# Kernel optimization log

Measured on AMD Instinct MI355X. Metric: run time of the kernel, lower is better.

Reference implementation:

```python
import jax, jax.numpy as jnp
import numpy as np

NUM_HEADS = 16
THETA = 10000.0


def _rope(x, cos, sin):
    # x: [B, H, S, d_k]; cos/sin: [S, d_k//2]
    x_even = x[..., 0::2]
    x_odd = x[..., 1::2]
    out_even = x_even * cos - x_odd * sin
    out_odd = x_odd * cos + x_even * sin
    # interleave back to original even/odd layout
    return jnp.stack([out_even, out_odd], axis=-1).reshape(x.shape)


def setup_inputs() -> dict:
    key = jax.random.key(0)
    ks = jax.random.split(key, 5)
    B, S, D = 2, 2048, 1024
    std = 2.0 / (D + D)
    return {
        "x": jax.random.normal(ks[0], (B, S, D), dtype=jnp.float32),
        "w_q": jax.random.normal(ks[1], (D, D), dtype=jnp.float32) * std,
        "w_k": jax.random.normal(ks[2], (D, D), dtype=jnp.float32) * std,
        "w_v": jax.random.normal(ks[3], (D, D), dtype=jnp.float32) * std,
        "w_o": jax.random.normal(ks[4], (D, D), dtype=jnp.float32) * std,
    }


def reference(x, w_q, w_k, w_v, w_o):
    B, S, D = x.shape
    H = NUM_HEADS
    d_k = D // H

    # QKV projections: x @ W.T
    q = jnp.einsum('bsd,ed->bse', x, w_q).reshape(B, S, H, d_k).transpose(0, 2, 1, 3)
    k = jnp.einsum('bsd,ed->bse', x, w_k).reshape(B, S, H, d_k).transpose(0, 2, 1, 3)
    v = jnp.einsum('bsd,ed->bse', x, w_v).reshape(B, S, H, d_k).transpose(0, 2, 1, 3)

    # RoPE (token_positions = arange(S))
    pos = jnp.arange(S, dtype=jnp.float32)
    inv_freq = 1.0 / (THETA ** (2.0 * jnp.arange(d_k // 2, dtype=jnp.float32) / d_k))
    angles = pos[:, None] * inv_freq[None, :]  # [S, d_k//2]
    cos, sin = jnp.cos(angles), jnp.sin(angles)
    q = _rope(q, cos, sin)
    k = _rope(k, cos, sin)

    # causal attention
    scores = jnp.einsum('bhqd,bhkd->bhqk', q, k) / jnp.sqrt(jnp.float32(d_k))
    causal = jnp.tril(jnp.ones((S, S), dtype=bool))
    scores = jnp.where(causal[None, None], scores, -jnp.inf)
    attn = jax.nn.softmax(scores, axis=-1)
    out = jnp.einsum('bhqk,bhkd->bhqd', attn, v)  # [B, H, S, d_k]

    out = out.transpose(0, 2, 1, 3).reshape(B, S, D)
    return jnp.einsum('bsd,ed->bse', out, w_o)
```

## Files before the change

kernel.cpp:

```cpp
#include <hip/hip_runtime.h>

typedef unsigned short u16;
typedef unsigned int u32;
typedef short bf16x8 __attribute__((ext_vector_type(8)));
typedef float f32x4 __attribute__((ext_vector_type(4)));

#define CSC 0.18033688011112042f

__device__ __forceinline__ u16 f2bf(float f) {
    union { float f; unsigned u; } x; x.f = f;
    unsigned r = x.u + 0x7fffu + ((x.u >> 16) & 1u);
    return (u16)(r >> 16);
}
__device__ __forceinline__ float bf2f(u16 v) {
    union { unsigned u; float f; } x; x.u = ((unsigned)v) << 16;
    return x.f;
}
__device__ __forceinline__ float exp2_fast(float x) {
#if __has_builtin(__builtin_amdgcn_exp2f)
    return __builtin_amdgcn_exp2f(x);
#else
    return exp2f(x);
#endif
}
__device__ __forceinline__ void gl_lds16(const u16* g, u16* l) {
#if __has_builtin(__builtin_amdgcn_global_load_lds)
    __builtin_amdgcn_global_load_lds(
        (const __attribute__((address_space(1))) unsigned int*)g,
        (__attribute__((address_space(3))) unsigned int*)l, 16, 0, 0);
#else
    *(bf16x8*)l = *(const bf16x8*)g;
#endif
}
__device__ __forceinline__ int ileave(int x) {
    return (x < 16) ? (x << 1) : (((x - 16) << 1) | 1);
}

__global__ void cvt_x_kernel(const float* __restrict__ in, u16* __restrict__ out, int n4) {
    int i = blockIdx.x * blockDim.x + threadIdx.x;
    if (i < n4) {
        float4 v = ((const float4*)in)[i];
        ushort4 o;
        o.x = f2bf(v.x); o.y = f2bf(v.y); o.z = f2bf(v.z); o.w = f2bf(v.w);
        ((ushort4*)out)[i] = o;
    }
}

__global__ void cvt_w_kernel(const float* __restrict__ wq, const float* __restrict__ wk,
                             const float* __restrict__ wv, const float* __restrict__ wo,
                             u16* __restrict__ qkvw, u16* __restrict__ ow) {
    int i = blockIdx.x * 256 + threadIdx.x;
    int m = blockIdx.y;
    const float* src = (m == 0) ? wq : (m == 1) ? wk : (m == 2) ? wv : wo;
    u16* dst = (m < 3) ? (qkvw + (size_t)m * 1048576) : ow;
    float4 v = ((const float4*)src)[i];
    ushort4 o;
    o.x = f2bf(v.x); o.y = f2bf(v.y); o.z = f2bf(v.z); o.w = f2bf(v.w);
    ((ushort4*)dst)[i] = o;
}

__global__ void rope_kernel(u16* __restrict__ qb, u16* __restrict__ kb) {
    int idx = blockIdx.x * 256 + threadIdx.x;
    u16* buf = blockIdx.y ? kb : qb;
    int i = idx & 31;
    int s = (idx >> 5) & 2047;
    float inv = exp2_fast((float)i * -0.4152410118609203f);
    float ang = (float)s * inv;
    float sn, cs;
    sincosf(ang, &sn, &cs);
    u16* p = buf + (size_t)(idx >> 5) * 64 + 2 * i;
    float e = bf2f(p[0]);
    float o = bf2f(p[1]);
    p[0] = f2bf(e * cs - o * sn);
    p[1] = f2bf(o * cs + e * sn);
}

__global__ __launch_bounds__(256) void gemm_qkv(const u16* __restrict__ A,
                                                const u16* __restrict__ Bw,
                                                u16* __restrict__ C, int K) {
    __shared__ __align__(16) u16 SH[8192];
    u16* As = SH;
    u16* Bs = SH + 4096;
    const int tid  = threadIdx.x;
    const int bm   = blockIdx.x * 128;
    const int bn   = blockIdx.y * 128;
    const int wave = tid >> 6, lane = tid & 63;
    const int wm   = (wave >> 1) * 64, wn = (wave & 1) * 64;
    const int l16  = lane & 15, quad = lane >> 4;
    const int mat  = bn >> 10;

    f32x4 acc[4][4];
    #pragma unroll
    for (int i = 0; i < 4; i++)
        #pragma unroll
        for (int j = 0; j < 4; j++)
            #pragma unroll
            for (int e = 0; e < 4; e++) acc[i][j][e] = 0.0f;

    const int srow = tid >> 2, scol = (tid & 3) * 8;
    const u16* gA0 = A  + (size_t)(bm + srow) * K + scol;
    const u16* gA1 = A  + (size_t)(bm + 64 + srow) * K + scol;
    const u16* gB0 = Bw + (size_t)(bn + srow) * K + scol;
    const u16* gB1 = Bw + (size_t)(bn + 64 + srow) * K + scol;
    u16* lA0 = &As[(size_t)tid * 8];
    u16* lA1 = &As[(size_t)(tid + 256) * 8];
    u16* lB0 = &Bs[(size_t)tid * 8];
    u16* lB1 = &Bs[(size_t)(tid + 256) * 8];

    for (int k0 = 0; k0 < K; k0 += 32) {
        __syncthreads();
        gl_lds16(gA0 + k0, lA0);
        gl_lds16(gA1 + k0, lA1);
        gl_lds16(gB0 + k0, lB0);
        gl_lds16(gB1 + k0, lB1);
        __syncthreads();
        bf16x8 af[4], bfr[4];
        #pragma unroll
        for (int i = 0; i < 4; i++) af[i]  = *(const bf16x8*)&As[(wm + i * 16 + l16) * 32 + quad * 8];
        #pragma unroll
        for (int j = 0; j < 4; j++) bfr[j] = *(const bf16x8*)&Bs[(wn + j * 16 + l16) * 32 + quad * 8];
        #pragma unroll
        for (int i = 0; i < 4; i++)
            #pragma unroll
            for (int j = 0; j < 4; j++)
                acc[i][j] = __builtin_amdgcn_mfma_f32_16x16x32_bf16(af[i], bfr[j], acc[i][j], 0, 0, 0);
    }

    if (mat < 2) {
        #pragma unroll
        for (int i = 0; i < 4; i++)
            #pragma unroll
            for (int j = 0; j < 4; j++)
                #pragma unroll
                for (int r = 0; r < 4; r++) {
                    int mr = bm + wm + i * 16 + quad * 4 + r;
                    int nc = bn + wn + j * 16 + l16;
                    int c = nc & 1023;
                    int b = mr >> 11, s = mr & 2047, h = c >> 6, dv = c & 63;
                    C[(size_t)mat * 4194304 + (((size_t)(b * 16 + h) * 2048 + s) * 64) + dv] =
                        f2bf(acc[i][j][r]);
                }
    } else {
        const int b  = bm >> 11, sb = bm & 2047;
        #pragma unroll
        for (int pass = 0; pass < 2; ++pass) {
            __syncthreads();
            if ((wn >> 6) == pass) {
                #pragma unroll
                for (int i = 0; i < 4; i++)
                    #pragma unroll
                    for (int j = 0; j < 4; j++)
                        #pragma unroll
                        for (int r = 0; r < 4; r++) {
                            int row = j * 16 + l16;
                            int ml  = wm + i * 16 + quad * 4 + r;
                            int sp  = (ml & ~31) | ileave(ml & 31);
                            SH[row * 128 + sp] = f2bf(acc[i][j][r]);
                        }
            }
            __syncthreads();
            int row = tid >> 2, seg = tid & 3;
            int cc  = (bn + pass * 64 + row) & 1023;
            int h = cc >> 6, dv = cc & 63;
            u16* dst = C + (size_t)8388608 +
                       (((size_t)(b * 16 + h) * 64 + dv) * 2048) + sb + seg * 32;
            const u16* srcp = &SH[row * 128 + seg * 32];
            #pragma unroll
            for (int kk = 0; kk < 4; ++kk)
                *(bf16x8*)(dst + kk * 8) = *(const bf16x8*)(srcp + kk * 8);
        }
    }
}

__global__ __launch_bounds__(256, 2) void gemm_out(const u16* __restrict__ A,
                                                   const u16* __restrict__ Bw,
                                                   float* __restrict__ C, int K) {
    __shared__ __align__(16) u16 As[128 * 32];
    __shared__ __align__(16) u16 Bs[64 * 32];
    const int tid  = threadIdx.x;
    const int bm   = blockIdx.x * 128;
    const int bn   = blockIdx.y * 64;
    const int wave = tid >> 6, lane = tid & 63;
    const int wm   = wave * 32;
    const int l16  = lane & 15, quad = lane >> 4;

    f32x4 acc[2][4];
    #pragma unroll
    for (int i = 0; i < 2; i++)
        #pragma unroll
        for (int j = 0; j < 4; j++)
            #pragma unroll
            for (int e = 0; e < 4; e++) acc[i][j][e] = 0.0f;

    const int srow = tid >> 2, scol = (tid & 3) * 8;
    const u16* gA0 = A  + (size_t)(bm + srow) * K + scol;
    const u16* gA1 = A  + (size_t)(bm + 64 + srow) * K + scol;
    const u16* gB0 = Bw + (size_t)(bn + srow) * K + scol;
    u16* lA0 = &As[(size_t)tid * 8];
    u16* lA1 = &As[(size_t)(tid + 256) * 8];
    u16* lB0 = &Bs[(size_t)tid * 8];

    for (int k0 = 0; k0 < K; k0 += 32) {
        __syncthreads();
        gl_lds16(gA0 + k0, lA0);
        gl_lds16(gA1 + k0, lA1);
        gl_lds16(gB0 + k0, lB0);
        __syncthreads();
        bf16x8 af[2], bfr[4];
        #pragma unroll
        for (int i = 0; i < 2; i++) af[i]  = *(const bf16x8*)&As[(wm + i * 16 + l16) * 32 + quad * 8];
        #pragma unroll
        for (int j = 0; j < 4; j++) bfr[j] = *(const bf16x8*)&Bs[(j * 16 + l16) * 32 + quad * 8];
        #pragma unroll
        for (int i = 0; i < 2; i++)
            #pragma unroll
            for (int j = 0; j < 4; j++)
                acc[i][j] = __builtin_amdgcn_mfma_f32_16x16x32_bf16(af[i], bfr[j], acc[i][j], 0, 0, 0);
    }

    #pragma unroll
    for (int i = 0; i < 2; i++)
        #pragma unroll
        for (int j = 0; j < 4; j++)
            #pragma unroll
            for (int r = 0; r < 4; r++) {
                int mr = bm + wm + i * 16 + quad * 4 + r;
                int nc = bn + j * 16 + l16;
                C[(size_t)mr * 1024 + nc] = acc[i][j][r];
            }
}

__global__ __launch_bounds__(256, 2) void attn_kernel(const u16* __restrict__ Q,
                                                      const u16* __restrict__ Kb,
                                                      const u16* __restrict__ Vt,
                                                      u16* __restrict__ Oout) {
    __shared__ __align__(16) u16 KV[8192];
    __shared__ __align__(16) u16 PW[4 * 1152];
    const int tid  = threadIdx.x;
    const int wave = tid >> 6, lane = tid & 63;
    const int l16  = lane & 15, quad = lane >> 4;
    const int j    = blockIdx.x;
    const int bh   = blockIdx.y;
    const int T    = 32 - j;
    const int qA0  = j * 64 + wave * 16;
    const int qB0  = (31 - j) * 64 + wave * 16;

    const u16* Qh = Q  + (size_t)bh * 2048 * 64;
    const u16* Kh = Kb + (size_t)bh * 2048 * 64;
    const u16* Vh = Vt + (size_t)bh * 64 * 2048;

    bf16x8 qAf0 = *(const bf16x8*)&Qh[(size_t)(qA0 + l16) * 64 + quad * 8];
    bf16x8 qAf1 = *(const bf16x8*)&Qh[(size_t)(qA0 + l16) * 64 + 32 + quad * 8];
    bf16x8 qBf0 = *(const bf16x8*)&Qh[(size_t)(qB0 + l16) * 64 + quad * 8];
    bf16x8 qBf1 = *(const bf16x8*)&Qh[(size_t)(qB0 + l16) * 64 + 32 + quad * 8];

    f32x4 oA[4], oB[4];
    float lsA[4], lsB[4];
    #pragma unroll
    for (int t = 0; t < 4; t++)
        #pragma unroll
        for (int e = 0; e < 4; e++) { oA[t][e] = 0.0f; oB[t][e] = 0.0f; }
    #pragma unroll
    for (int r = 0; r < 4; r++) { lsA[r] = 0.0f; lsB[r] = 0.0f; }

    const int cch = tid;
    const u16* gK = Kh + (size_t)(cch >> 2) * 64 + (cch & 3) * 8;
    const u16* gV = Vh + (size_t)(cch >> 2) * 2048 + (cch & 3) * 8;
    u16* lK0 = &KV[(size_t)cch * 8];
    u16* lK1 = &KV[2048 + (size_t)cch * 8];
    u16* lV0 = &KV[4096 + (size_t)cch * 8];
    u16* lV1 = &KV[6144 + (size_t)cch * 8];

    u16* pw16 = PW + wave * 1152;
    u32* pw32 = (u32*)pw16;

    auto side = [&](const bf16x8& q0f, const bf16x8& q1f, bf16x8* kf0, bf16x8* kf1,
                    bf16x8* vf0, bf16x8* vf1, f32x4* o, float* ls,
                    int q0, int kbase, bool diag) {
        f32x4 s[4];
        #pragma unroll
        for (int n = 0; n < 4; n++) {
            #pragma unroll
            for (int e = 0; e < 4; e++) s[n][e] = 0.0f;
            s[n] = __builtin_amdgcn_mfma_f32_16x16x32_bf16(q0f, kf0[n], s[n], 0, 0, 0);
            s[n] = __builtin_amdgcn_mfma_f32_16x16x32_bf16(q1f, kf1[n], s[n], 0, 0, 0);
        }
        float p[4][4];
        #pragma unroll
        for (int n = 0; n < 4; n++)
            #pragma unroll
            for (int r = 0; r < 4; r++) {
                float v = exp2_fast(s[n][r] * CSC);
                if (diag) {
                    int row = q0 + quad * 4 + r;
                    v = (kbase + n * 16 + l16 > row) ? 0.0f : v;
                }
                p[n][r] = v;
                ls[r] += v;
            }
        #pragma unroll
        for (int c = 0; c < 2; c++)
            #pragma unroll
            for (int r = 0; r < 4; r++)
                pw32[(quad * 4 + r) * 36 + c * 16 + l16] =
                    (u32)f2bf(p[2 * c][r]) | ((u32)f2bf(p[2 * c + 1][r]) << 16);
        asm volatile("s_waitcnt lgkmcnt(0)" ::: "memory");
        bf16x8 pf0 = *(const bf16x8*)&pw16[l16 * 72 + quad * 8];
        bf16x8 pf1 = *(const bf16x8*)&pw16[l16 * 72 + 32 + quad * 8];
        #pragma unroll
        for (int dn = 0; dn < 4; dn++) {
            o[dn] = __builtin_amdgcn_mfma_f32_16x16x32_bf16(pf0, vf0[dn], o[dn], 0, 0, 0);
            o[dn] = __builtin_amdgcn_mfma_f32_16x16x32_bf16(pf1, vf1[dn], o[dn], 0, 0, 0);
        }
    };

    for (int t = 0; t < T; ++t) {
        __syncthreads();
        gl_lds16(gK + (size_t)t * 4096, lK0);
        gl_lds16(gK + (size_t)t * 4096 + 32, lK1);
        gl_lds16(gV + (size_t)t * 64, lV0);
        gl_lds16(gV + (size_t)t * 64 + 32, lV1);
        __syncthreads();

        bf16x8 kf0[4], kf1[4], vf0[4], vf1[4];
        #pragma unroll
        for (int n = 0; n < 4; n++) {
            int ri = (n * 16 + l16) * 32 + quad * 8;
            kf0[n] = *(const bf16x8*)&KV[ri];
            kf1[n] = *(const bf16x8*)&KV[2048 + ri];
            vf0[n] = *(const bf16x8*)&KV[4096 + ri];
            vf1[n] = *(const bf16x8*)&KV[6144 + ri];
        }
        const int kbase = t * 64;
        side(qBf0, qBf1, kf0, kf1, vf0, vf1, oB, lsB, qB0, kbase, t == T - 1);
        if (t <= j)
            side(qAf0, qAf1, kf0, kf1, vf0, vf1, oA, lsA, qA0, kbase, t == j);
    }

    #pragma unroll
    for (int off = 1; off < 16; off <<= 1)
        #pragma unroll
        for (int r = 0; r < 4; r++) {
            lsA[r] += __shfl_xor(lsA[r], off);
            lsB[r] += __shfl_xor(lsB[r], off);
        }

    const int b = bh >> 4, h = bh & 15;
    #pragma unroll
    for (int r = 0; r < 4; r++) {
        float iA = 1.0f / lsA[r];
        float iB = 1.0f / lsB[r];
        int sA = qA0 + quad * 4 + r;
        int sB = qB0 + quad * 4 + r;
        #pragma unroll
        for (int dn = 0; dn < 4; dn++) {
            int d = h * 64 + dn * 16 + l16;
            Oout[((size_t)b * 2048 + sA) * 1024 + d] = f2bf(oA[dn][r] * iA);
            Oout[((size_t)b * 2048 + sB) * 1024 + d] = f2bf(oB[dn][r] * iB);
        }
    }
}

extern "C" void kernel_launch(void* const* d_in, const int* in_sizes, int n_in,
                              void* d_out, int out_size, void* d_ws, size_t ws_size,
                              hipStream_t stream) {
    const float* x  = (const float*)d_in[0];
    const float* wq = (const float*)d_in[1];
    const float* wk = (const float*)d_in[2];
    const float* wv = (const float*)d_in[3];
    const float* wo = (const float*)d_in[4];
    float* out = (float*)d_out;

    const int M = 4096, D = 1024;
    u16* xb    = (u16*)d_ws;
    u16* qkvw  = xb   + (size_t)M * D;
    u16* ow    = qkvw + (size_t)3 * D * D;
    u16* qkv   = ow   + (size_t)D * D;
    u16* qb    = qkv;
    u16* kb    = qkv + (size_t)M * D;
    u16* vtb   = qkv + (size_t)2 * M * D;
    u16* aob   = qkv + (size_t)3 * M * D;

    cvt_x_kernel<<<(M * D / 4 + 255) / 256, 256, 0, stream>>>(x, xb, M * D / 4);
    dim3 gw(D * D / 4 / 256, 4);
    cvt_w_kernel<<<gw, 256, 0, stream>>>(wq, wk, wv, wo, qkvw, ow);

    dim3 gq(32, 24);
    gemm_qkv<<<gq, 256, 0, stream>>>(xb, qkvw, qkv, D);

    dim3 gr(32 * 2048 * 32 / 256, 2);
    rope_kernel<<<gr, 256, 0, stream>>>(qb, kb);

    dim3 ga(16, 32);
    attn_kernel<<<ga, 256, 0, stream>>>(qb, kb, vtb, aob);

    dim3 go(32, 16);
    gemm_out<<<go, 256, 0, stream>>>(aob, ow, out, D);
}
```

Measured before the change: 199.5 us.

## Double-buffer attention K/V, fuse conversion kernels, vectorize RoPE and coalesce QKV stores

Merges the x and weight fp32-to-bf16 conversions into one launch and vectorizes RoPE to 8 elements per thread, folding the softmax scale into Q during RoPE. The Q/K epilogue of the QKV GEMM now goes through padded LDS for coalesced 16-byte stores, and the V transpose buffer is padded to cut bank conflicts. The attention kernel double-buffers K/V tiles in LDS so the next tile loads while the current one computes, and it remaps block indices to change scheduling order. These changes add LDS usage, which may lower occupancy, and the attention loop drops the second barrier, so correctness depends on the async global-to-LDS loads finishing before the next iteration's barrier.

```diff
diff --git a/kernel.cpp b/kernel.cpp
--- a/kernel.cpp
+++ b/kernel.cpp
@@ -36,49 +36,62 @@
     return (x < 16) ? (x << 1) : (((x - 16) << 1) | 1);
 }
 
-__global__ void cvt_x_kernel(const float* __restrict__ in, u16* __restrict__ out, int n4) {
-    int i = blockIdx.x * blockDim.x + threadIdx.x;
-    if (i < n4) {
-        float4 v = ((const float4*)in)[i];
-        ushort4 o;
-        o.x = f2bf(v.x); o.y = f2bf(v.y); o.z = f2bf(v.z); o.w = f2bf(v.w);
-        ((ushort4*)out)[i] = o;
-    }
-}
-
-__global__ void cvt_w_kernel(const float* __restrict__ wq, const float* __restrict__ wk,
-                             const float* __restrict__ wv, const float* __restrict__ wo,
-                             u16* __restrict__ qkvw, u16* __restrict__ ow) {
+__global__ void cvt_all_kernel(const float* __restrict__ x, const float* __restrict__ wq,
+                               const float* __restrict__ wk, const float* __restrict__ wv,
+                               const float* __restrict__ wo,
+                               u16* __restrict__ xb, u16* __restrict__ qkvw,
+                               u16* __restrict__ ow) {
     int i = blockIdx.x * 256 + threadIdx.x;
-    int m = blockIdx.y;
-    const float* src = (m == 0) ? wq : (m == 1) ? wk : (m == 2) ? wv : wo;
-    u16* dst = (m < 3) ? (qkvw + (size_t)m * 1048576) : ow;
-    float4 v = ((const float4*)src)[i];
+    const float4* src;
+    ushort4* dst;
+    if (i < 1048576) {
+        src = (const float4*)x + i;
+        dst = (ushort4*)xb + i;
+    } else {
+        int r = i - 1048576;
+        int m = r >> 18;
+        int off = r & 262143;
+        const float* s4 = (m == 0) ? wq : (m == 1) ? wk : (m == 2) ? wv : wo;
+        u16* d = (m < 3) ? (qkvw + (size_t)m * 1048576) : ow;
+        src = (const float4*)s4 + off;
+        dst = (ushort4*)d + off;
+    }
+    float4 v = *src;
     ushort4 o;
     o.x = f2bf(v.x); o.y = f2bf(v.y); o.z = f2bf(v.z); o.w = f2bf(v.w);
-    ((ushort4*)dst)[i] = o;
+    *dst = o;
 }
 
 __global__ void rope_kernel(u16* __restrict__ qb, u16* __restrict__ kb) {
     int idx = blockIdx.x * 256 + threadIdx.x;
-    u16* buf = blockIdx.y ? kb : qb;
-    int i = idx & 31;
-    int s = (idx >> 5) & 2047;
-    float inv = exp2_fast((float)i * -0.4152410118609203f);
-    float ang = (float)s * inv;
-    float sn, cs;
-    sincosf(ang, &sn, &cs);
-    u16* p = buf + (size_t)(idx >> 5) * 64 + 2 * i;
-    float e = bf2f(p[0]);
-    float o = bf2f(p[1]);
-    p[0] = f2bf(e * cs - o * sn);
-    p[1] = f2bf(o * cs + e * sn);
+    u16* buf;
+    float scale;
+    if (blockIdx.y == 0) { buf = qb; scale = CSC; } else { buf = kb; scale = 1.0f; }
+    int g   = idx & 7;
+    int row = idx >> 3;
+    int s   = row & 2047;
+    u16* p = buf + (size_t)row * 64 + g * 8;
+    bf16x8 v = *(bf16x8*)p;
+    bf16x8 o;
+    #pragma unroll
+    for (int q = 0; q < 4; ++q) {
+        int i = g * 4 + q;
+        float inv = exp2_fast((float)i * -0.4152410118609203f);
+        float ang = (float)s * inv;
+        float sn, cs;
+        sincosf(ang, &sn, &cs);
+        float e  = bf2f(((u16*)&v)[2 * q]);
+        float od = bf2f(((u16*)&v)[2 * q + 1]);
+        ((u16*)&o)[2 * q]     = f2bf((e * cs - od * sn) * scale);
+        ((u16*)&o)[2 * q + 1] = f2bf((od * cs + e * sn) * scale);
+    }
+    *(bf16x8*)p = o;
 }
 
 __global__ __launch_bounds__(256) void gemm_qkv(const u16* __restrict__ A,
                                                 const u16* __restrict__ Bw,
                                                 u16* __restrict__ C, int K) {
-    __shared__ __align__(16) u16 SH[8192];
+    __shared__ __align__(16) u16 SH[8448];
     u16* As = SH;
     u16* Bs = SH + 4096;
     const int tid  = threadIdx.x;
@@ -126,22 +139,37 @@
                 acc[i][j] = __builtin_amdgcn_mfma_f32_16x16x32_bf16(af[i], bfr[j], acc[i][j], 0, 0, 0);
     }
 
+    const int b  = bm >> 11, sb = bm & 2047;
     if (mat < 2) {
         #pragma unroll
-        for (int i = 0; i < 4; i++)
-            #pragma unroll
-            for (int j = 0; j < 4; j++)
+        for (int pass = 0; pass < 2; ++pass) {
+            __syncthreads();
+            if ((wn >> 6) == pass) {
                 #pragma unroll
-                for (int r = 0; r < 4; r++) {
-                    int mr = bm + wm + i * 16 + quad * 4 + r;
-                    int nc = bn + wn + j * 16 + l16;
-                    int c = nc & 1023;
-                    int b = mr >> 11, s = mr & 2047, h = c >> 6, dv = c & 63;
-                    C[(size_t)mat * 4194304 + (((size_t)(b * 16 + h) * 2048 + s) * 64) + dv] =
-                        f2bf(acc[i][j][r]);
-                }
+                for (int i = 0; i < 4; i++)
+                    #pragma unroll
+                    for (int j = 0; j < 4; j++)
+                        #pragma unroll
+                        for (int r = 0; r < 4; r++) {
+                            int rl = wm + i * 16 + quad * 4 + r;
+                            int cl = j * 16 + l16;
+                            SH[rl * 66 + cl] = f2bf(acc[i][j][r]);
+                        }
+            }
+            __syncthreads();
+            int rl   = tid >> 1;
+            int half = (tid & 1) * 32;
+            int c    = (bn + pass * 64) & 1023;
+            int h    = c >> 6;
+            int s    = sb + rl;
+            u16* dst = C + (size_t)mat * 4194304 +
+                       (((size_t)(b * 16 + h) * 2048 + s) * 64) + half;
+            const u16* srcp = &SH[rl * 66 + half];
+            #pragma unroll
+            for (int kk = 0; kk < 4; ++kk)
+                *(bf16x8*)(dst + kk * 8) = *(const bf16x8*)(srcp + kk * 8);
+        }
     } else {
-        const int b  = bm >> 11, sb = bm & 2047;
         #pragma unroll
         for (int pass = 0; pass < 2; ++pass) {
             __syncthreads();
@@ -155,7 +183,7 @@
                             int row = j * 16 + l16;
                             int ml  = wm + i * 16 + quad * 4 + r;
                             int sp  = (ml & ~31) | ileave(ml & 31);
-                            SH[row * 128 + sp] = f2bf(acc[i][j][r]);
+                            SH[row * 130 + sp] = f2bf(acc[i][j][r]);
                         }
             }
             __syncthreads();
@@ -164,7 +192,7 @@
             int h = cc >> 6, dv = cc & 63;
             u16* dst = C + (size_t)8388608 +
                        (((size_t)(b * 16 + h) * 64 + dv) * 2048) + sb + seg * 32;
-            const u16* srcp = &SH[row * 128 + seg * 32];
+            const u16* srcp = &SH[row * 130 + seg * 32];
             #pragma unroll
             for (int kk = 0; kk < 4; ++kk)
                 *(bf16x8*)(dst + kk * 8) = *(const bf16x8*)(srcp + kk * 8);
@@ -234,13 +262,14 @@
                                                       const u16* __restrict__ Kb,
                                                       const u16* __restrict__ Vt,
                                                       u16* __restrict__ Oout) {
-    __shared__ __align__(16) u16 KV[8192];
+    __shared__ __align__(16) u16 KV[2][8192];
     __shared__ __align__(16) u16 PW[4 * 1152];
     const int tid  = threadIdx.x;
     const int wave = tid >> 6, lane = tid & 63;
     const int l16  = lane & 15, quad = lane >> 4;
-    const int j    = blockIdx.x;
-    const int bh   = blockIdx.y;
+    const int bid  = blockIdx.x;
+    const int j    = (bid >> 3) & 15;
+    const int bh   = (bid & 7) * 4 + (bid >> 7);
     const int T    = 32 - j;
     const int qA0  = j * 64 + wave * 16;
     const int qB0  = (31 - j) * 64 + wave * 16;
@@ -263,16 +292,19 @@
     #pragma unroll
     for (int r = 0; r < 4; r++) { lsA[r] = 0.0f; lsB[r] = 0.0f; }
 
-    const int cch = tid;
-    const u16* gK = Kh + (size_t)(cch >> 2) * 64 + (cch & 3) * 8;
-    const u16* gV = Vh + (size_t)(cch >> 2) * 2048 + (cch & 3) * 8;
-    u16* lK0 = &KV[(size_t)cch * 8];
-    u16* lK1 = &KV[2048 + (size_t)cch * 8];
-    u16* lV0 = &KV[4096 + (size_t)cch * 8];
-    u16* lV1 = &KV[6144 + (size_t)cch * 8];
+    const u16* gK = Kh + (size_t)(tid >> 2) * 64 + (tid & 3) * 8;
+    const u16* gV = Vh + (size_t)(tid >> 2) * 2048 + (tid & 3) * 8;
 
     u16* pw16 = PW + wave * 1152;
     u32* pw32 = (u32*)pw16;
+
+    auto stage = [&](int t, int buf) {
+        u16* base = KV[buf];
+        gl_lds16(gK + (size_t)t * 4096,      base + (size_t)tid * 8);
+        gl_lds16(gK + (size_t)t * 4096 + 32, base + 2048 + (size_t)tid * 8);
+        gl_lds16(gV + (size_t)t * 64,        base + 4096 + (size_t)tid * 8);
+        gl_lds16(gV + (size_t)t * 64 + 32,   base + 6144 + (size_t)tid * 8);
+    };
 
     auto side = [&](const bf16x8& q0f, const bf16x8& q1f, bf16x8* kf0, bf16x8* kf1,
                     bf16x8* vf0, bf16x8* vf1, f32x4* o, float* ls,
@@ -290,7 +322,7 @@
         for (int n = 0; n < 4; n++)
             #pragma unroll
             for (int r = 0; r < 4; r++) {
-                float v = exp2_fast(s[n][r] * CSC);
+                float v = exp2_fast(s[n][r]);
                 if (diag) {
                     int row = q0 + quad * 4 + r;
                     v = (kbase + n * 16 + l16 > row) ? 0.0f : v;
@@ -314,22 +346,19 @@
         }
     };
 
+    stage(0, 0);
     for (int t = 0; t < T; ++t) {
         __syncthreads();
-        gl_lds16(gK + (size_t)t * 4096, lK0);
-        gl_lds16(gK + (size_t)t * 4096 + 32, lK1);
-        gl_lds16(gV + (size_t)t * 64, lV0);
-        gl_lds16(gV + (size_t)t * 64 + 32, lV1);
-        __syncthreads();
-
+        if (t + 1 < T) stage(t + 1, (t + 1) & 1);
+        const u16* B = KV[t & 1];
         bf16x8 kf0[4], kf1[4], vf0[4], vf1[4];
         #pragma unroll
         for (int n = 0; n < 4; n++) {
             int ri = (n * 16 + l16) * 32 + quad * 8;
-            kf0[n] = *(const bf16x8*)&KV[ri];
-            kf1[n] = *(const bf16x8*)&KV[2048 + ri];
-            vf0[n] = *(const bf16x8*)&KV[4096 + ri];
-            vf1[n] = *(const bf16x8*)&KV[6144 + ri];
+            kf0[n] = *(const bf16x8*)&B[ri];
+            kf1[n] = *(const bf16x8*)&B[2048 + ri];
+            vf0[n] = *(const bf16x8*)&B[4096 + ri];
+            vf1[n] = *(const bf16x8*)&B[6144 + ri];
         }
         const int kbase = t * 64;
         side(qBf0, qBf1, kf0, kf1, vf0, vf1, oB, lsB, qB0, kbase, t == T - 1);
@@ -381,18 +410,15 @@
     u16* vtb   = qkv + (size_t)2 * M * D;
     u16* aob   = qkv + (size_t)3 * M * D;
 
-    cvt_x_kernel<<<(M * D / 4 + 255) / 256, 256, 0, stream>>>(x, xb, M * D / 4);
-    dim3 gw(D * D / 4 / 256, 4);
-    cvt_w_kernel<<<gw, 256, 0, stream>>>(wq, wk, wv, wo, qkvw, ow);
+    cvt_all_kernel<<<8192, 256, 0, stream>>>(x, wq, wk, wv, wo, xb, qkvw, ow);
 
     dim3 gq(32, 24);
     gemm_qkv<<<gq, 256, 0, stream>>>(xb, qkvw, qkv, D);
 
-    dim3 gr(32 * 2048 * 32 / 256, 2);
+    dim3 gr(2048, 2);
     rope_kernel<<<gr, 256, 0, stream>>>(qb, kb);
 
-    dim3 ga(16, 32);
-    attn_kernel<<<ga, 256, 0, stream>>>(qb, kb, vtb, aob);
+    attn_kernel<<<512, 256, 0, stream>>>(qb, kb, vtb, aob);
 
     dim3 go(32, 16);
     gemm_out<<<go, 256, 0, stream>>>(aob, ow, out, D);
```

Result: no change. 198.9 us (-0.3%).
